# Kernel optimization log

Hardware: AMD Instinct MI355X
Metric: run time of the kernel (lower is better)

Reference implementation:

```python
import jax, jax.numpy as jnp
import numpy as np

# init_kwargs constants
MIN_T = 0.01
MAX_T = 0.5
TGT_MIN = 0.005
TGT_MAX = 0.03
W_MIN = 15.0
W_MAX = 5.0
W_CONT = 5.0
W_SIZE = 7.0
LESION_T = 0.3


def setup_inputs() -> dict:
    key = jax.random.key(0)
    pred = jax.random.uniform(key, (16, 1, 128, 128, 128), dtype=jnp.float32)
    return {"pred": pred}


def reference(pred):
    # pred: [B, 1, D, H, W]
    s = pred[:, 0]  # [B, D, H, W]
    B = s.shape[0]
    axes = (1, 2, 3)

    # -- min/max activation penalties (per-sample threshold means) --
    act = jnp.mean((s > MIN_T).astype(s.dtype), axis=axes)          # [B]
    loss = jax.nn.relu(TGT_MIN - act) * W_MIN
    high = jnp.mean((s > MAX_T).astype(s.dtype), axis=axes)
    loss = loss + jax.nn.relu(high - TGT_MAX) * W_MAX

    # -- continuity penalty: mean abs finite differences along D,H,W --
    d_grad = jnp.mean(jnp.abs(s[:, 1:] - s[:, :-1]), axis=axes)
    h_grad = jnp.mean(jnp.abs(s[:, :, 1:] - s[:, :, :-1]), axis=axes)
    w_grad = jnp.mean(jnp.abs(s[:, :, :, 1:] - s[:, :, :, :-1]), axis=axes)
    avg_grad = (d_grad + h_grad + w_grad) / 3.0
    has_lesion = jnp.any(s > LESION_T, axis=axes)
    loss = loss + jnp.where(has_lesion, jnp.minimum(avg_grad, 1.0), 0.0) * W_CONT

    # -- size-variance penalty over masked active values (unbiased std, torch.std) --
    mask = (s > MIN_T).astype(s.dtype)
    cnt = jnp.sum(mask, axis=axes)                                   # [B]
    cnt_safe = jnp.maximum(cnt, 1.0)
    m = jnp.sum(s * mask, axis=axes) / cnt_safe                      # masked mean [B]
    sq = jnp.sum(mask * (s - m[:, None, None, None]) ** 2, axis=axes)
    gate = (act > 0.001) & (cnt > 1.0)
    var = jnp.where(gate, sq / jnp.maximum(cnt - 1.0, 1.0), 1.0)     # guard sqrt/grad when gated off
    std = jnp.sqrt(var)
    rel_std = std / (m + 1e-6)
    pen = jnp.exp(-5.0 * rel_std)
    loss = loss + jnp.where(gate, pen, 0.0) * W_SIZE

    return jnp.sum(loss) / B
```

## Files before the change

### kernel.cpp

```cpp
#include <hip/hip_runtime.h>
#include <math.h>

#define MIN_T    0.01f
#define MAX_T    0.5f
#define LESION_T 0.3f

constexpr int NB       = 16;
constexpr int DIM      = 128;
constexpr int PLANE_F4 = DIM * DIM / 4;
constexpr int VOX      = DIM * DIM * DIM;
constexpr int THREADS  = 256;
constexpr int HWBLKS   = PLANE_F4 / THREADS;
constexpr int DSEGS    = 8;
constexpr int DPS      = DIM / DSEGS;
constexpr int NACC     = 8;

__global__ __launch_bounds__(THREADS, 8)
void partial_kernel(const float* __restrict__ pred, double* __restrict__ acc)
{
    const int seg   = blockIdx.x;
    const int hwblk = blockIdx.y;
    const int b     = blockIdx.z;
    const int tid   = (int)threadIdx.x;

    const float4* __restrict__ s4 =
        reinterpret_cast<const float4*>(pred + (size_t)b * VOX);

    const int  h    = hwblk * 8 + (tid >> 5);
    const bool do_h = (h < DIM - 1);
    const bool do_w = ((tid & 31) != 31);

    const int d0    = seg * DPS;
    const int npair = (seg == DSEGS - 1) ? (DPS - 1) : DPS;
    const int last  = d0 + npair;

    float cnt_min = 0.f, cnt_max = 0.f, sum_d = 0.f, sum_h = 0.f,
          sum_w = 0.f, sm = 0.f, sm2 = 0.f, les = 0.f;

    auto process = [&](const float4& v, const float4& vh) {
        const float xs[4] = { v.x, v.y, v.z, v.w };
        #pragma unroll
        for (int j = 0; j < 4; ++j) {
            const float x    = xs[j];
            const bool  gmin = (x > MIN_T);
            const float xm   = gmin ? x : 0.0f;
            cnt_min += gmin ? 1.0f : 0.0f;
            sm      += xm;
            sm2      = fmaf(xm, x, sm2);
            cnt_max += (x > MAX_T)    ? 1.0f : 0.0f;
            les     += (x > LESION_T) ? 1.0f : 0.0f;
        }
        sum_w += fabsf(v.y - v.x) + fabsf(v.z - v.y) + fabsf(v.w - v.z);
        const float nx = __shfl_down(v.x, 1, 64);
        if (do_w) sum_w += fabsf(nx - v.w);
        if (do_h) sum_h += fabsf(vh.x - v.x) + fabsf(vh.y - v.y)
                         + fabsf(vh.z - v.z) + fabsf(vh.w - v.w);
    };

    const float4 z4 = { 0.f, 0.f, 0.f, 0.f };
    const size_t off = (size_t)hwblk * THREADS + tid;
    size_t base = (size_t)d0 * PLANE_F4 + off;
    const size_t lastbase = (size_t)last * PLANE_F4 + off;

    float4 v0 = s4[base];
    float4 h0 = do_h ? s4[base + 32] : z4;
    float4 v1 = s4[base + PLANE_F4];
    float4 h1 = do_h ? s4[base + PLANE_F4 + 32] : z4;
    size_t pbase = base + 2 * (size_t)PLANE_F4;

    for (int d = d0; d < d0 + npair; ++d) {
        const size_t pf = (pbase < lastbase) ? pbase : lastbase;
        const float4 v2 = s4[pf];
        const float4 h2 = do_h ? s4[pf + 32] : z4;
        process(v0, h0);
        sum_d += fabsf(v1.x - v0.x) + fabsf(v1.y - v0.y)
               + fabsf(v1.z - v0.z) + fabsf(v1.w - v0.w);
        v0 = v1; h0 = h1; v1 = v2; h1 = h2;
        pbase += PLANE_F4;
    }
    if (seg == DSEGS - 1)
        process(v0, h0);

    float vals[NACC] = { cnt_min, cnt_max, sum_d, sum_h, sum_w, sm, sm2, les };
    #pragma unroll
    for (int vi = 0; vi < NACC; ++vi) {
        float x = vals[vi];
        #pragma unroll
        for (int offs = 32; offs > 0; offs >>= 1)
            x += __shfl_down(x, offs, 64);
        vals[vi] = x;
    }

    __shared__ float smem[4][NACC];
    const int wave = tid >> 6;
    const int lane = tid & 63;
    if (lane == 0) {
        #pragma unroll
        for (int vi = 0; vi < NACC; ++vi) smem[wave][vi] = vals[vi];
    }
    __syncthreads();
    if (tid < NACC) {
        const float t = smem[0][tid] + smem[1][tid] +
                        smem[2][tid] + smem[3][tid];
        atomicAdd(&acc[(size_t)b * NACC + tid], (double)t);
    }
}

__global__ __launch_bounds__(64)
void finalize_kernel(const double* __restrict__ acc, float* __restrict__ out)
{
    float l = 0.0f;
    if (threadIdx.x < NB) {
        const double* a = acc + (size_t)threadIdx.x * NACC;
        const double cnt    = a[0];
        const double cntmax = a[1];
        const double sd     = a[2];
        const double sh     = a[3];
        const double sw     = a[4];
        const double sm     = a[5];
        const double sm2    = a[6];
        const double les    = a[7];

        const double inv_vox = 1.0 / (double)VOX;
        const double act  = cnt    * inv_vox;
        const double high = cntmax * inv_vox;

        double loss = fmax(0.005 - act, 0.0) * 15.0
                    + fmax(high - 0.03, 0.0) * 5.0;

        const double grad_den = 127.0 * 128.0 * 128.0;
        const double avg_grad = (sd + sh + sw) / (3.0 * grad_den);
        if (les > 0.5)
            loss += fmin(avg_grad, 1.0) * 5.0;

        const double cnt_safe = fmax(cnt, 1.0);
        const double m  = sm / cnt_safe;
        double sq = sm2 - 2.0 * m * sm + m * m * cnt;
        if (sq < 0.0) sq = 0.0;

        const bool gate = (act > 0.001) && (cnt > 1.0);
        if (gate) {
            const double var     = sq / fmax(cnt - 1.0, 1.0);
            const double rel_std = sqrt(var) / (m + 1e-6);
            loss += exp(-5.0 * rel_std) * 7.0;
        }
        l = (float)loss;
    }
    #pragma unroll
    for (int offs = 32; offs > 0; offs >>= 1)
        l += __shfl_down(l, offs, 64);
    if (threadIdx.x == 0)
        out[0] = l / (float)NB;
}

extern "C" void kernel_launch(void* const* d_in, const int* in_sizes, int n_in,
                              void* d_out, int out_size, void* d_ws, size_t ws_size,
                              hipStream_t stream)
{
    const float* pred = (const float*)d_in[0];
    float* out        = (float*)d_out;
    double* acc       = (double*)d_ws;

    hipMemsetAsync(d_ws, 0, (size_t)NB * NACC * sizeof(double), stream);

    dim3 grid(DSEGS, HWBLKS, NB);
    partial_kernel<<<grid, THREADS, 0, stream>>>(pred, acc);
    finalize_kernel<<<1, 64, 0, stream>>>(acc, out);
}
```

Before: 193.8 us.

## Fuse finalize into partial kernel via last-block counter and float atomics

Merges the finalize kernel into the partial-reduction kernel. A global atomic counter lets the last block to finish compute the loss, which removes one kernel launch. The per-sample accumulators switch from double to float atomics, which are cheaper, and the occupancy hint in launch_bounds is dropped. The risks are float precision loss in large sums (sm2 and counts near 1.6M per sample can round) and nondeterministic summation order.

```diff
diff --git a/kernel.cpp b/kernel.cpp
--- a/kernel.cpp
+++ b/kernel.cpp
@@ -14,9 +14,11 @@
 constexpr int DSEGS    = 8;
 constexpr int DPS      = DIM / DSEGS;
 constexpr int NACC     = 8;
+constexpr int TOTAL_BLOCKS = DSEGS * HWBLKS * NB;
 
-__global__ __launch_bounds__(THREADS, 8)
-void partial_kernel(const float* __restrict__ pred, double* __restrict__ acc)
+__global__ __launch_bounds__(THREADS)
+void fused_kernel(const float* __restrict__ pred, float* __restrict__ acc,
+                  unsigned* __restrict__ counter, float* __restrict__ out)
 {
     const int seg   = blockIdx.x;
     const int hwblk = blockIdx.y;
@@ -99,27 +101,38 @@
         for (int vi = 0; vi < NACC; ++vi) smem[wave][vi] = vals[vi];
     }
     __syncthreads();
+
+    __shared__ unsigned lastflag;
     if (tid < NACC) {
         const float t = smem[0][tid] + smem[1][tid] +
                         smem[2][tid] + smem[3][tid];
-        atomicAdd(&acc[(size_t)b * NACC + tid], (double)t);
+        atomicAdd(&acc[b * NACC + tid], t);
     }
-}
+    __syncthreads();
+    if (tid == 0) {
+        __threadfence();
+        const unsigned old = atomicAdd(counter, 1u);
+        lastflag = (old == TOTAL_BLOCKS - 1) ? 1u : 0u;
+    }
+    __syncthreads();
+    if (!lastflag) return;
 
-__global__ __launch_bounds__(64)
-void finalize_kernel(const double* __restrict__ acc, float* __restrict__ out)
-{
-    float l = 0.0f;
-    if (threadIdx.x < NB) {
-        const double* a = acc + (size_t)threadIdx.x * NACC;
+    __shared__ float sacc[NB * NACC];
+    __shared__ float lss[NB];
+    if (tid < NB * NACC)
+        sacc[tid] = atomicAdd(&acc[tid], 0.0f);
+    __syncthreads();
+
+    if (tid < NB) {
+        const float* a = &sacc[tid * NACC];
         const double cnt    = a[0];
         const double cntmax = a[1];
         const double sd     = a[2];
         const double sh     = a[3];
         const double sw     = a[4];
-        const double sm     = a[5];
-        const double sm2    = a[6];
-        const double les    = a[7];
+        const double smv    = a[5];
+        const double sm2v   = a[6];
+        const double lescnt = a[7];
 
         const double inv_vox = 1.0 / (double)VOX;
         const double act  = cnt    * inv_vox;
@@ -130,12 +143,12 @@
 
         const double grad_den = 127.0 * 128.0 * 128.0;
         const double avg_grad = (sd + sh + sw) / (3.0 * grad_den);
-        if (les > 0.5)
+        if (lescnt > 0.5)
             loss += fmin(avg_grad, 1.0) * 5.0;
 
         const double cnt_safe = fmax(cnt, 1.0);
-        const double m  = sm / cnt_safe;
-        double sq = sm2 - 2.0 * m * sm + m * m * cnt;
+        const double m  = smv / cnt_safe;
+        double sq = sm2v - 2.0 * m * smv + m * m * cnt;
         if (sq < 0.0) sq = 0.0;
 
         const bool gate = (act > 0.001) && (cnt > 1.0);
@@ -144,13 +157,15 @@
             const double rel_std = sqrt(var) / (m + 1e-6);
             loss += exp(-5.0 * rel_std) * 7.0;
         }
-        l = (float)loss;
+        lss[tid] = (float)loss;
     }
-    #pragma unroll
-    for (int offs = 32; offs > 0; offs >>= 1)
-        l += __shfl_down(l, offs, 64);
-    if (threadIdx.x == 0)
-        out[0] = l / (float)NB;
+    __syncthreads();
+    if (tid == 0) {
+        float s = 0.f;
+        #pragma unroll
+        for (int i = 0; i < NB; ++i) s += lss[i];
+        out[0] = s / (float)NB;
+    }
 }
 
 extern "C" void kernel_launch(void* const* d_in, const int* in_sizes, int n_in,
@@ -159,11 +174,11 @@
 {
     const float* pred = (const float*)d_in[0];
     float* out        = (float*)d_out;
-    double* acc       = (double*)d_ws;
+    float* acc        = (float*)d_ws;
+    unsigned* counter = (unsigned*)((char*)d_ws + NB * NACC * sizeof(float));
 
-    hipMemsetAsync(d_ws, 0, (size_t)NB * NACC * sizeof(double), stream);
+    hipMemsetAsync(d_ws, 0, NB * NACC * sizeof(float) + sizeof(unsigned), stream);
 
     dim3 grid(DSEGS, HWBLKS, NB);
-    partial_kernel<<<grid, THREADS, 0, stream>>>(pred, acc);
-    finalize_kernel<<<1, 64, 0, stream>>>(acc, out);
+    fused_kernel<<<grid, THREADS, 0, stream>>>(pred, acc, counter, out);
 }
```

Measured after the change: 265.1 us. +36.8%, slower.
